# Performance work log

Measured on AMD Instinct MI355X. Metric: run time of the kernel, lower is better.

The kernel has to match this reference:

```python
import jax, jax.numpy as jnp
import numpy as np

SIGMA_E, SIGMA_I, K_E, K_I = 0.6, 1.2, 0.8, 1.0
PM_STEPS, DT, BETA = 4, 0.15, 1.0
EPS = 1e-4


def setup_inputs() -> dict:
    key = jax.random.key(0)
    ks = jax.random.split(key, 12)
    B, d_in, d_lat, ch, d_out, n_c = 4096, 784, 8, 32, 10, 16
    inp = {
        "x": jax.random.normal(ks[0], (B, d_in), dtype=jnp.float32),
        "W1": jax.random.normal(ks[1], (d_in, 128), dtype=jnp.float32) * 0.03,
        "b1": jnp.zeros((128,), jnp.float32),
        "W2": jax.random.normal(ks[2], (128, d_lat), dtype=jnp.float32) * 0.08,
        "b2": jnp.zeros((d_lat,), jnp.float32),
        "centers": jax.random.normal(ks[3], (n_c, d_lat), dtype=jnp.float32) * 0.7,
        "mus": jnp.ones((n_c,), jnp.float32) * 0.5,
        "Wp": jax.random.normal(ks[4], (d_lat, ch), dtype=jnp.float32) * 0.3,
        "bp": jnp.zeros((ch,), jnp.float32),
        "Wr": jax.random.normal(ks[5], (ch, d_out), dtype=jnp.float32) * 0.15,
        "br": jnp.zeros((d_out,), jnp.float32),
        "T": 5,
    }
    return inp


def grad_ln_n(z, centers, mus):
    # z: [B,d], centers: [C,d], mus: [C]
    rvec = z[:, None, :] - centers[None, :, :]          # [B,C,d]
    r = jnp.sqrt(jnp.sum(rvec * rvec, axis=-1) + EPS)   # [B,C]
    n = 1.0 + jnp.sum(mus[None, :] / r, axis=1)          # [B]
    g = -jnp.sum((mus[None, :] / (r ** 3))[:, :, None] * rvec, axis=1)  # [B,d]
    return g / n[:, None]


def pm_field(z, centers, mus):
    for _ in range(PM_STEPS):
        z = jnp.clip(z + DT * BETA * grad_ln_n(z, centers, mus), -3.0, 3.0)
    return z


def lateral_kernel(z):
    # squared pairwise distances via the norm trick (avoids [B,B,d])
    sq = jnp.sum(z * z, axis=1)
    dist2 = jnp.maximum(sq[:, None] + sq[None, :] - 2.0 * (z @ z.T), 0.0)
    K = K_E * jnp.exp(-dist2 / (2.0 * SIGMA_E ** 2)) - K_I * jnp.exp(-dist2 / (2.0 * SIGMA_I ** 2))
    return jax.lax.stop_gradient(K)  # torch.no_grad in original


def reference(x, W1, b1, W2, b2, centers, mus, Wp, bp, Wr, br, T):
    B = x.shape[0]
    z = jnp.tanh(x.reshape(B, -1) @ W1 + b1) @ W2 + b2   # encoder
    h = jnp.zeros((B, Wr.shape[0]), x.dtype)
    for _ in range(T):
        z = pm_field(z, centers, mus)
        h = 0.9 * h + 0.1 * jnp.tanh(z @ Wp + bp)
        h = h + 0.05 * (lateral_kernel(z) @ h)
        y = h @ Wr + br
    return y
```

## Files before the change

### kernel.cpp

```cpp
#include <hip/hip_runtime.h>
#include <math.h>

#define NB    4096
#define DIN   784
#define DH    128
#define DL    8
#define NC    16
#define NCH   32
#define DO    10
#define TSTEPS 5

#define KH_ROWS   64
#define KH_TILE   64
#define KH_JSLICE 256
#define KH_P      (NB / KH_JSLICE)


__global__ __launch_bounds__(256) void enc1_kernel(const float* __restrict__ x,
    const float* __restrict__ W1, double* __restrict__ P)
{
    __shared__ float xsT[56][18];
    __shared__ float wss[56][128];
    const int tid = threadIdx.x;
    const int m0 = blockIdx.x * 16;
    const int kbeg = blockIdx.y * 392;
    const int cg = tid & 31, rg = tid >> 5;
    const int c0 = cg << 2, r0 = rg << 1;
    double acc[2][4] = {};
    for (int it = 0; it < 7; ++it) {
        const int k0 = kbeg + it * 56;
        __syncthreads();
        if (tid < 224) {
            int row = tid / 14, f = tid % 14;
            float4 v = *(const float4*)(x + (m0 + row) * DIN + k0 + f * 4);
            int kk = f * 4;
            xsT[kk][row] = v.x; xsT[kk + 1][row] = v.y;
            xsT[kk + 2][row] = v.z; xsT[kk + 3][row] = v.w;
        }
        for (int l = tid; l < 56 * 32; l += 256) {
            int kk = l >> 5, c = (l & 31) << 2;
            *(float4*)&wss[kk][c] = *(const float4*)(W1 + (k0 + kk) * DH + c);
        }
        __syncthreads();
#pragma unroll 8
        for (int kk = 0; kk < 56; ++kk) {
            const float2 xv = *(const float2*)&xsT[kk][r0];
            const float4 wv = *(const float4*)&wss[kk][c0];
            const double x0 = (double)xv.x, x1 = (double)xv.y;
            const double w0 = (double)wv.x, w1 = (double)wv.y;
            const double w2v = (double)wv.z, w3 = (double)wv.w;
            acc[0][0] += x0 * w0; acc[0][1] += x0 * w1;
            acc[0][2] += x0 * w2v; acc[0][3] += x0 * w3;
            acc[1][0] += x1 * w0; acc[1][1] += x1 * w1;
            acc[1][2] += x1 * w2v; acc[1][3] += x1 * w3;
        }
    }
    double* Pr = P + (size_t)blockIdx.y * (NB * DH);
#pragma unroll
    for (int i = 0; i < 2; ++i) {
        double* dst = Pr + (m0 + r0 + i) * DH + c0;
        *(double2*)dst       = make_double2(acc[i][0], acc[i][1]);
        *(double2*)(dst + 2) = make_double2(acc[i][2], acc[i][3]);
    }
}

__global__ __launch_bounds__(256) void enc2_kernel(const double* __restrict__ P,
    const float* __restrict__ b1, const float* __restrict__ W2,
    const float* __restrict__ b2, double* __restrict__ zbuf)
{
    __shared__ double As[16][132];
    __shared__ double W2d[DH * DL];
    const int tid = threadIdx.x;
    const int m0 = blockIdx.x * 16;
    for (int l = tid; l < DH * DL; l += 256) W2d[l] = (double)W2[l];
    for (int l = tid; l < 16 * 128; l += 256) {
        int row = l >> 7, k = l & 127;
        double v = P[(m0 + row) * DH + k] + P[(size_t)NB * DH + (m0 + row) * DH + k]
                 + (double)b1[k];
        As[row][k] = tanh(v);
    }
    __syncthreads();
    const int row = tid >> 4, d = (tid >> 1) & 7, half = tid & 1;
    double a = 0.0;
#pragma unroll 8
    for (int i = 0; i < 64; ++i) {
        const int k = half + (i << 1);
        a += As[row][k] * W2d[k * 8 + d];
    }
    a += __shfl_xor(a, 1);
    if (half == 0) zbuf[(m0 + row) * DL + d] = a + (double)b2[d];
}

__global__ __launch_bounds__(256) void enc_fused_kernel(const float* __restrict__ x,
    const float* __restrict__ W1, const float* __restrict__ b1,
    const float* __restrict__ W2, const float* __restrict__ b2,
    double* __restrict__ zbuf)
{
    __shared__ float  xsT[56][9];
    __shared__ float  wss[56][128];
    __shared__ double Asd[8][131];
    __shared__ double W2d[DH * DL];
    const int tid = threadIdx.x;
    const int m0 = blockIdx.x * 8;
    const int cg = tid & 31, rg = tid >> 5;
    const int c0 = cg << 2;
    for (int l = tid; l < DH * DL; l += 256) W2d[l] = (double)W2[l];
    double acc[4] = {};
    for (int it = 0; it < 14; ++it) {
        const int k0 = it * 56;
        __syncthreads();
        if (tid < 112) {
            int row = tid / 14, f = tid % 14;
            float4 v = *(const float4*)(x + (m0 + row) * DIN + k0 + f * 4);
            int kk = f * 4;
            xsT[kk][row] = v.x; xsT[kk + 1][row] = v.y;
            xsT[kk + 2][row] = v.z; xsT[kk + 3][row] = v.w;
        }
        for (int l = tid; l < 56 * 32; l += 256) {
            int kk = l >> 5, c = (l & 31) << 2;
            *(float4*)&wss[kk][c] = *(const float4*)(W1 + (k0 + kk) * DH + c);
        }
        __syncthreads();
#pragma unroll 8
        for (int kk = 0; kk < 56; ++kk) {
            const double xv = (double)xsT[kk][rg];
            const float4 wv = *(const float4*)&wss[kk][c0];
            acc[0] += xv * (double)wv.x;
            acc[1] += xv * (double)wv.y;
            acc[2] += xv * (double)wv.z;
            acc[3] += xv * (double)wv.w;
        }
    }
    __syncthreads();
#pragma unroll
    for (int j = 0; j < 4; ++j)
        Asd[rg][c0 + j] = tanh(acc[j] + (double)b1[c0 + j]);
    __syncthreads();
    {
        const int row = tid >> 5, d = (tid >> 2) & 7, kq = tid & 3;
        double a = 0.0;
#pragma unroll 8
        for (int i = 0; i < 32; ++i) {
            const int k = kq + (i << 2);
            a += Asd[row][k] * W2d[k * 8 + d];
        }
        a += __shfl_xor(a, 1);
        a += __shfl_xor(a, 2);
        if (kq == 0) zbuf[(m0 + row) * DL + d] = a + (double)b2[d];
    }
}

__global__ __launch_bounds__(256) void pmh_kernel(double* __restrict__ zbuf,
    const float* __restrict__ centers, const float* __restrict__ mus,
    const float* __restrict__ Wp, const float* __restrict__ bp,
    double* __restrict__ hB, float* __restrict__ zf, float* __restrict__ sqf,
    float* __restrict__ hAf, const float* __restrict__ part, int first)
{
    const int tid = threadIdx.x;
    const int lane = tid & 15;
    const int s = tid >> 4;
    const int i = blockIdx.x * 16 + s;
    double cz[8];
#pragma unroll
    for (int d = 0; d < 8; ++d) cz[d] = (double)centers[lane * DL + d];
    const double mu = (double)mus[lane];
    double z[8];
#pragma unroll
    for (int p = 0; p < 4; ++p) {
        double2 v = *(const double2*)(zbuf + i * DL + p * 2);
        z[p * 2] = v.x; z[p * 2 + 1] = v.y;
    }
#pragma unroll
    for (int st = 0; st < 4; ++st) {
        double rv[8];
        double ss = 1e-4;
#pragma unroll
        for (int d = 0; d < 8; ++d) { rv[d] = z[d] - cz[d]; ss += rv[d] * rv[d]; }
        double r = sqrt(ss);
        double mr = mu / r;
        double n = mr;
        double mr3 = mr / ss;
        double g[8];
#pragma unroll
        for (int d = 0; d < 8; ++d) g[d] = -mr3 * rv[d];
#pragma unroll
        for (int m = 1; m < 16; m <<= 1) {
            n += __shfl_xor(n, m);
#pragma unroll
            for (int d = 0; d < 8; ++d) g[d] += __shfl_xor(g[d], m);
        }
        double sc = 0.15 / (1.0 + n);
#pragma unroll
        for (int d = 0; d < 8; ++d) z[d] = fmin(3.0, fmax(-3.0, z[d] + sc * g[d]));
    }
    if (lane == 0) {
        double sq = 0.0;
#pragma unroll
        for (int d = 0; d < 8; ++d) sq += z[d] * z[d];
        sqf[i] = (float)sq;
#pragma unroll
        for (int p = 0; p < 4; ++p)
            *(double2*)(zbuf + i * DL + p * 2) = make_double2(z[p * 2], z[p * 2 + 1]);
        float4 a = make_float4((float)z[0], (float)z[1], (float)z[2], (float)z[3]);
        float4 b = make_float4((float)z[4], (float)z[5], (float)z[6], (float)z[7]);
        *(float4*)(zf + i * DL)     = a;
        *(float4*)(zf + i * DL + 4) = b;
    }
#pragma unroll
    for (int cc = 0; cc < 2; ++cc) {
        const int c = lane + cc * 16;
        double a = (double)bp[c];
#pragma unroll
        for (int d = 0; d < 8; ++d) a += z[d] * (double)Wp[d * NCH + c];
        double ph = tanh(a);
        double prev = 0.0;
        if (!first) {
            prev = hB[i * NCH + c];
            if (part) {
                double sp = 0.0;
#pragma unroll
                for (int p = 0; p < KH_P; ++p)
                    sp += (double)part[(size_t)p * (NB * NCH) + i * NCH + c];
                prev += 0.05 * sp;
            }
        }
        double hv = 0.9 * prev + 0.1 * ph;
        hAf[i * NCH + c] = (float)hv;
        hB[i * NCH + c] = hv;
    }
}

__global__ __launch_bounds__(256) void kh_kernel(const float* __restrict__ zf,
    const float* __restrict__ sqf, const float* __restrict__ hAf,
    double* __restrict__ hB, float* __restrict__ part)
{
    __shared__ float zjs[KH_TILE][8];
    __shared__ float sqjs[KH_TILE];
    __shared__ float hs[KH_TILE][32];
    __shared__ float redA[KH_ROWS][33];
    __shared__ float redB[KH_ROWS][33];
    const int tid = threadIdx.x;
    const int wave = tid >> 6, lane = tid & 63;
    const int row = blockIdx.x * KH_ROWS + lane;
    const int j_base = blockIdx.y * KH_JSLICE;
    float zr[8];
    {
        float4 a = *(const float4*)(zf + row * 8);
        float4 b = *(const float4*)(zf + row * 8 + 4);
        zr[0] = a.x; zr[1] = a.y; zr[2] = a.z; zr[3] = a.w;
        zr[4] = b.x; zr[5] = b.y; zr[6] = b.z; zr[7] = b.w;
    }
    const float my_sq = sqf[row];
    const float invI = 1.0f / 2.88f;
    const float invE = 1.0f / 0.72f;
    float acc[32] = {};
    for (int jt = 0; jt < KH_JSLICE / KH_TILE; ++jt) {
        const int j0 = j_base + jt * KH_TILE;
        __syncthreads();
        {
            int jj = tid >> 2, p = (tid & 3) << 1;
            *(float2*)&zjs[jj][p] = *(const float2*)(zf + (j0 + jj) * 8 + p);
        }
        if (tid < KH_TILE) sqjs[tid] = sqf[j0 + tid];
        for (int l = tid; l < KH_TILE * 8; l += 256) {
            int jh = l >> 3, p = (l & 7) << 2;
            *(float4*)&hs[jh][p] = *(const float4*)(hAf + (j0 + jh) * NCH + p);
        }
        __syncthreads();
        const int jjbeg = wave * 16;
#pragma unroll 2
        for (int q = 0; q < 16; ++q) {
            const int jj = jjbeg + q;
            const float4 a = *(const float4*)&zjs[jj][0];
            const float4 b = *(const float4*)&zjs[jj][4];
            float dot = zr[0] * a.x + zr[1] * a.y + zr[2] * a.z + zr[3] * a.w
                      + zr[4] * b.x + zr[5] * b.y + zr[6] * b.z + zr[7] * b.w;
            float d2 = fmaxf(my_sq + sqjs[jj] - 2.0f * dot, 0.0f);
            float K = 0.8f * __expf(-d2 * invE) - __expf(-d2 * invI);
#pragma unroll
            for (int c = 0; c < 32; c += 4) {
                const float4 hv = *(const float4*)&hs[jj][c];
                acc[c]     += K * hv.x;
                acc[c + 1] += K * hv.y;
                acc[c + 2] += K * hv.z;
                acc[c + 3] += K * hv.w;
            }
        }
    }
    __syncthreads();
    if (wave == 1) {
#pragma unroll
        for (int c = 0; c < 32; ++c) redA[lane][c] = acc[c];
    } else if (wave == 3) {
#pragma unroll
        for (int c = 0; c < 32; ++c) redB[lane][c] = acc[c];
    }
    __syncthreads();
    if (wave == 0) {
#pragma unroll
        for (int c = 0; c < 32; ++c) acc[c] += redA[lane][c];
    } else if (wave == 2) {
#pragma unroll
        for (int c = 0; c < 32; ++c) acc[c] += redB[lane][c];
    }
    __syncthreads();
    if (wave == 2) {
#pragma unroll
        for (int c = 0; c < 32; ++c) redA[lane][c] = acc[c];
    }
    __syncthreads();
    if (wave == 0) {
#pragma unroll
        for (int c = 0; c < 32; ++c) acc[c] += redA[lane][c];
        if (part) {
            float* pr = part + (size_t)blockIdx.y * (NB * NCH) + row * NCH;
#pragma unroll
            for (int c = 0; c < 32; c += 4)
                *(float4*)(pr + c) = make_float4(acc[c], acc[c + 1], acc[c + 2], acc[c + 3]);
        } else {
#pragma unroll
            for (int c = 0; c < 32; ++c)
                atomicAdd(&hB[row * NCH + c], 0.05 * (double)acc[c]);
        }
    }
}

__global__ __launch_bounds__(256) void y_kernel(const double* __restrict__ h,
    const float* __restrict__ part, const float* __restrict__ Wr,
    const float* __restrict__ br, float* __restrict__ y)
{
    __shared__ double hsy[16][33];
    __shared__ double wrs[NCH * DO];
    __shared__ double brs[DO];
    const int tid = threadIdx.x;
    const int rb = blockIdx.x * 16;
    for (int l = tid; l < 16 * 32; l += 256) {
        int row = l >> 5, k = l & 31;
        const int gi = (rb + row) * NCH + k;
        double v = h[gi];
        if (part) {
            double sp = 0.0;
#pragma unroll
            for (int p = 0; p < KH_P; ++p) sp += (double)part[(size_t)p * (NB * NCH) + gi];
            v += 0.05 * sp;
        }
        hsy[row][k] = v;
    }
    for (int l = tid; l < NCH * DO; l += 256) wrs[l] = (double)Wr[l];
    if (tid < DO) brs[tid] = (double)br[tid];
    __syncthreads();
    const int row = tid >> 4, col = tid & 15;
    if (col < DO) {
        double a = brs[col];
#pragma unroll
        for (int k = 0; k < NCH; ++k) a += hsy[row][k] * wrs[k * DO + col];
        y[(rb + row) * DO + col] = (float)a;
    }
}

extern "C" void kernel_launch(void* const* d_in, const int* in_sizes, int n_in,
                              void* d_out, int out_size, void* d_ws, size_t ws_size,
                              hipStream_t stream)
{
    const float* x   = (const float*)d_in[0];
    const float* W1  = (const float*)d_in[1];
    const float* b1  = (const float*)d_in[2];
    const float* W2  = (const float*)d_in[3];
    const float* b2  = (const float*)d_in[4];
    const float* cen = (const float*)d_in[5];
    const float* mus = (const float*)d_in[6];
    const float* Wp  = (const float*)d_in[7];
    const float* bp  = (const float*)d_in[8];
    const float* Wr  = (const float*)d_in[9];
    const float* br  = (const float*)d_in[10];

    float* y = (float*)d_out;
    double* zbuf = (double*)d_ws;
    double* hB   = zbuf + NB * DL;
    float*  zf   = (float*)(hB + NB * NCH);
    float*  sqf  = zf + NB * DL;
    float*  hAf  = sqf + NB;
    float*  part = hAf + NB * NCH;
    double* Penc = (double*)(part + (size_t)KH_P * NB * NCH);

    const size_t need_part = (size_t)(NB * DL + NB * NCH) * 8
                           + (size_t)(NB * DL + NB + NB * NCH + KH_P * NB * NCH) * 4;
    const size_t need_full = need_part + (size_t)2 * NB * DH * 8;
    float* pp = (ws_size >= need_part) ? part : (float*)nullptr;

    if (ws_size >= need_full) {
        enc1_kernel<<<dim3(NB / 16, 2), 256, 0, stream>>>(x, W1, Penc);
        enc2_kernel<<<NB / 16, 256, 0, stream>>>(Penc, b1, W2, b2, zbuf);
    } else {
        enc_fused_kernel<<<NB / 8, 256, 0, stream>>>(x, W1, b1, W2, b2, zbuf);
    }
    for (int t = 0; t < TSTEPS; ++t) {
        pmh_kernel<<<NB / 16, 256, 0, stream>>>(zbuf, cen, mus, Wp, bp, hB,
                                                zf, sqf, hAf, pp, t == 0 ? 1 : 0);
        kh_kernel<<<dim3(NB / KH_ROWS, KH_P), 256, 0, stream>>>(zf, sqf, hAf, hB, pp);
    }
    y_kernel<<<NB / 16, 256, 0, stream>>>(hB, pp, Wr, br, y);
}
```

Before: 348.3 us.

## Split encoder K seven ways, register-block kh rows, cheapen exps and tanh

The encoder GEMM's K dimension is now split seven ways instead of two, giving more blocks, and enc2 sums seven partials. The kh kernel handles two rows per thread (128 rows per block), so each shared-memory z/h tile load is reused across twice as many rows. It also derives the excitatory exponential from the inhibitory one by raising it to the fourth power, which saves one exp. The PM step uses rsqrt in place of sqrt and divides, and the tanh in pmh runs in float. The costs are higher register pressure in kh, a larger partial-sum workspace for the encoder that may push it onto the fused fallback path, and reduced precision in tanh.

Result: no change. 353.7 us (+1.5%).

```diff
diff --git a/kernel.cpp b/kernel.cpp
--- a/kernel.cpp
+++ b/kernel.cpp
@@ -10,10 +10,11 @@
 #define DO    10
 #define TSTEPS 5
 
-#define KH_ROWS   64
+#define KH_ROWS   128
 #define KH_TILE   64
 #define KH_JSLICE 256
 #define KH_P      (NB / KH_JSLICE)
+#define ENC_G     7
 
 
 __global__ __launch_bounds__(256) void enc1_kernel(const float* __restrict__ x,
@@ -23,11 +24,11 @@
     __shared__ float wss[56][128];
     const int tid = threadIdx.x;
     const int m0 = blockIdx.x * 16;
-    const int kbeg = blockIdx.y * 392;
+    const int kbeg = blockIdx.y * 112;
     const int cg = tid & 31, rg = tid >> 5;
     const int c0 = cg << 2, r0 = rg << 1;
     double acc[2][4] = {};
-    for (int it = 0; it < 7; ++it) {
+    for (int it = 0; it < 2; ++it) {
         const int k0 = kbeg + it * 56;
         __syncthreads();
         if (tid < 224) {
@@ -75,8 +76,10 @@
     for (int l = tid; l < DH * DL; l += 256) W2d[l] = (double)W2[l];
     for (int l = tid; l < 16 * 128; l += 256) {
         int row = l >> 7, k = l & 127;
-        double v = P[(m0 + row) * DH + k] + P[(size_t)NB * DH + (m0 + row) * DH + k]
-                 + (double)b1[k];
+        double v = (double)b1[k];
+#pragma unroll
+        for (int s = 0; s < ENC_G; ++s)
+            v += P[(size_t)s * NB * DH + (m0 + row) * DH + k];
         As[row][k] = tanh(v);
     }
     __syncthreads();
@@ -176,10 +179,10 @@
         double ss = 1e-4;
 #pragma unroll
         for (int d = 0; d < 8; ++d) { rv[d] = z[d] - cz[d]; ss += rv[d] * rv[d]; }
-        double r = sqrt(ss);
-        double mr = mu / r;
+        double rinv = rsqrt(ss);
+        double mr = mu * rinv;
         double n = mr;
-        double mr3 = mr / ss;
+        double mr3 = mr * (rinv * rinv);
         double g[8];
 #pragma unroll
         for (int d = 0; d < 8; ++d) g[d] = -mr3 * rv[d];
@@ -212,7 +215,7 @@
         double a = (double)bp[c];
 #pragma unroll
         for (int d = 0; d < 8; ++d) a += z[d] * (double)Wp[d * NCH + c];
-        double ph = tanh(a);
+        double ph = (double)tanhf((float)a);
         double prev = 0.0;
         if (!first) {
             prev = hB[i * NCH + c];
@@ -237,23 +240,26 @@
     __shared__ float zjs[KH_TILE][8];
     __shared__ float sqjs[KH_TILE];
     __shared__ float hs[KH_TILE][32];
-    __shared__ float redA[KH_ROWS][33];
-    __shared__ float redB[KH_ROWS][33];
+    __shared__ float bufA[KH_ROWS][33];
+    __shared__ float bufB[KH_ROWS][33];
     const int tid = threadIdx.x;
     const int wave = tid >> 6, lane = tid & 63;
-    const int row = blockIdx.x * KH_ROWS + lane;
+    const int row0 = blockIdx.x * KH_ROWS + lane;
     const int j_base = blockIdx.y * KH_JSLICE;
-    float zr[8];
+    float zr0[8], zr1[8];
     {
-        float4 a = *(const float4*)(zf + row * 8);
-        float4 b = *(const float4*)(zf + row * 8 + 4);
-        zr[0] = a.x; zr[1] = a.y; zr[2] = a.z; zr[3] = a.w;
-        zr[4] = b.x; zr[5] = b.y; zr[6] = b.z; zr[7] = b.w;
-    }
-    const float my_sq = sqf[row];
+        float4 a = *(const float4*)(zf + row0 * 8);
+        float4 b = *(const float4*)(zf + row0 * 8 + 4);
+        zr0[0] = a.x; zr0[1] = a.y; zr0[2] = a.z; zr0[3] = a.w;
+        zr0[4] = b.x; zr0[5] = b.y; zr0[6] = b.z; zr0[7] = b.w;
+        float4 c = *(const float4*)(zf + (row0 + 64) * 8);
+        float4 d = *(const float4*)(zf + (row0 + 64) * 8 + 4);
+        zr1[0] = c.x; zr1[1] = c.y; zr1[2] = c.z; zr1[3] = c.w;
+        zr1[4] = d.x; zr1[5] = d.y; zr1[6] = d.z; zr1[7] = d.w;
+    }
+    const float sq0 = sqf[row0], sq1 = sqf[row0 + 64];
     const float invI = 1.0f / 2.88f;
-    const float invE = 1.0f / 0.72f;
-    float acc[32] = {};
+    float acc0[32] = {}, acc1[32] = {};
     for (int jt = 0; jt < KH_JSLICE / KH_TILE; ++jt) {
         const int j0 = j_base + jt * KH_TILE;
         __syncthreads();
@@ -273,54 +279,66 @@
             const int jj = jjbeg + q;
             const float4 a = *(const float4*)&zjs[jj][0];
             const float4 b = *(const float4*)&zjs[jj][4];
-            float dot = zr[0] * a.x + zr[1] * a.y + zr[2] * a.z + zr[3] * a.w
-                      + zr[4] * b.x + zr[5] * b.y + zr[6] * b.z + zr[7] * b.w;
-            float d2 = fmaxf(my_sq + sqjs[jj] - 2.0f * dot, 0.0f);
-            float K = 0.8f * __expf(-d2 * invE) - __expf(-d2 * invI);
+            const float sqj = sqjs[jj];
+            float dot0 = zr0[0] * a.x + zr0[1] * a.y + zr0[2] * a.z + zr0[3] * a.w
+                       + zr0[4] * b.x + zr0[5] * b.y + zr0[6] * b.z + zr0[7] * b.w;
+            float dot1 = zr1[0] * a.x + zr1[1] * a.y + zr1[2] * a.z + zr1[3] * a.w
+                       + zr1[4] * b.x + zr1[5] * b.y + zr1[6] * b.z + zr1[7] * b.w;
+            float d20 = fmaxf(sq0 + sqj - 2.0f * dot0, 0.0f);
+            float d21 = fmaxf(sq1 + sqj - 2.0f * dot1, 0.0f);
+            float e0 = __expf(-d20 * invI), e1 = __expf(-d21 * invI);
+            float t0 = e0 * e0, t1 = e1 * e1;
+            float K0 = 0.8f * (t0 * t0) - e0;
+            float K1 = 0.8f * (t1 * t1) - e1;
 #pragma unroll
             for (int c = 0; c < 32; c += 4) {
                 const float4 hv = *(const float4*)&hs[jj][c];
-                acc[c]     += K * hv.x;
-                acc[c + 1] += K * hv.y;
-                acc[c + 2] += K * hv.z;
-                acc[c + 3] += K * hv.w;
+                acc0[c]     += K0 * hv.x; acc0[c + 1] += K0 * hv.y;
+                acc0[c + 2] += K0 * hv.z; acc0[c + 3] += K0 * hv.w;
+                acc1[c]     += K1 * hv.x; acc1[c + 1] += K1 * hv.y;
+                acc1[c + 2] += K1 * hv.z; acc1[c + 3] += K1 * hv.w;
             }
         }
     }
     __syncthreads();
     if (wave == 1) {
 #pragma unroll
-        for (int c = 0; c < 32; ++c) redA[lane][c] = acc[c];
+        for (int c = 0; c < 32; ++c) { bufA[lane][c] = acc0[c]; bufA[lane + 64][c] = acc1[c]; }
     } else if (wave == 3) {
 #pragma unroll
-        for (int c = 0; c < 32; ++c) redB[lane][c] = acc[c];
+        for (int c = 0; c < 32; ++c) { bufB[lane][c] = acc0[c]; bufB[lane + 64][c] = acc1[c]; }
     }
     __syncthreads();
     if (wave == 0) {
 #pragma unroll
-        for (int c = 0; c < 32; ++c) acc[c] += redA[lane][c];
+        for (int c = 0; c < 32; ++c) { acc0[c] += bufA[lane][c]; acc1[c] += bufA[lane + 64][c]; }
     } else if (wave == 2) {
 #pragma unroll
-        for (int c = 0; c < 32; ++c) acc[c] += redB[lane][c];
+        for (int c = 0; c < 32; ++c) { acc0[c] += bufB[lane][c]; acc1[c] += bufB[lane + 64][c]; }
     }
     __syncthreads();
     if (wave == 2) {
 #pragma unroll
-        for (int c = 0; c < 32; ++c) redA[lane][c] = acc[c];
+        for (int c = 0; c < 32; ++c) { bufA[lane][c] = acc0[c]; bufA[lane + 64][c] = acc1[c]; }
     }
     __syncthreads();
     if (wave == 0) {
 #pragma unroll
-        for (int c = 0; c < 32; ++c) acc[c] += redA[lane][c];
+        for (int c = 0; c < 32; ++c) { acc0[c] += bufA[lane][c]; acc1[c] += bufA[lane + 64][c]; }
         if (part) {
-            float* pr = part + (size_t)blockIdx.y * (NB * NCH) + row * NCH;
-#pragma unroll
-            for (int c = 0; c < 32; c += 4)
-                *(float4*)(pr + c) = make_float4(acc[c], acc[c + 1], acc[c + 2], acc[c + 3]);
+            float* p0 = part + (size_t)blockIdx.y * (NB * NCH) + row0 * NCH;
+            float* p1 = p0 + 64 * NCH;
+#pragma unroll
+            for (int c = 0; c < 32; c += 4) {
+                *(float4*)(p0 + c) = make_float4(acc0[c], acc0[c + 1], acc0[c + 2], acc0[c + 3]);
+                *(float4*)(p1 + c) = make_float4(acc1[c], acc1[c + 1], acc1[c + 2], acc1[c + 3]);
+            }
         } else {
 #pragma unroll
-            for (int c = 0; c < 32; ++c)
-                atomicAdd(&hB[row * NCH + c], 0.05 * (double)acc[c]);
+            for (int c = 0; c < 32; ++c) {
+                atomicAdd(&hB[row0 * NCH + c], 0.05 * (double)acc0[c]);
+                atomicAdd(&hB[(row0 + 64) * NCH + c], 0.05 * (double)acc1[c]);
+            }
         }
     }
 }
@@ -385,11 +403,11 @@
 
     const size_t need_part = (size_t)(NB * DL + NB * NCH) * 8
                            + (size_t)(NB * DL + NB + NB * NCH + KH_P * NB * NCH) * 4;
-    const size_t need_full = need_part + (size_t)2 * NB * DH * 8;
+    const size_t need_full = need_part + (size_t)ENC_G * NB * DH * 8;
     float* pp = (ws_size >= need_part) ? part : (float*)nullptr;
 
     if (ws_size >= need_full) {
-        enc1_kernel<<<dim3(NB / 16, 2), 256, 0, stream>>>(x, W1, Penc);
+        enc1_kernel<<<dim3(NB / 16, ENC_G), 256, 0, stream>>>(x, W1, Penc);
         enc2_kernel<<<NB / 16, 256, 0, stream>>>(Penc, b1, W2, b2, zbuf);
     } else {
         enc_fused_kernel<<<NB / 8, 256, 0, stream>>>(x, W1, b1, W2, b2, zbuf);
```
